# Performance work log

Measured on AMD Instinct MI355X. Metric: run time of the kernel, lower is better.

The kernel has to match this reference:

```python
import jax, jax.numpy as jnp
import numpy as np

T, B, D, H = 1024, 8, 1024, 16
HD = D // H  # head_dim = 64


def setup_inputs() -> dict:
    key = jax.random.key(0)
    ks = jax.random.split(key, 11)
    s = 1.0 / np.sqrt(D)
    return {
        "query": jax.random.normal(ks[0], (T, B, D), jnp.float32),
        "key": jax.random.normal(ks[1], (T, B, D), jnp.float32),
        "value": jax.random.normal(ks[2], (T, B, D), jnp.float32),
        "Wq": jax.random.normal(ks[3], (D, D), jnp.float32) * s,
        "bq": jax.random.normal(ks[4], (D,), jnp.float32) * s,
        "Wk": jax.random.normal(ks[5], (D, D), jnp.float32) * s,
        "bk": jax.random.normal(ks[6], (D,), jnp.float32) * s,
        "Wv": jax.random.normal(ks[7], (D, D), jnp.float32) * s,
        "bv": jax.random.normal(ks[8], (D,), jnp.float32) * s,
        "Wo": jax.random.normal(ks[9], (D, D), jnp.float32) * s,
        "bo": jax.random.normal(ks[10], (D,), jnp.float32) * s,
    }


def reference(query, key, value, Wq, bq, Wk, bk, Wv, bv, Wo, bo):
    # query/key/value: (T, B, D) seq-first, as in nn.MultiheadAttention
    t, b, d = query.shape
    scale = HD ** -0.5
    # projections (torch Linear: x @ W.T + b), split into heads -> (B, H, T, HD)
    q = (query @ Wq.T + bq).reshape(t, b, H, HD).transpose(1, 2, 0, 3)
    k = (key @ Wk.T + bk).reshape(t, b, H, HD).transpose(1, 2, 0, 3)
    v = (value @ Wv.T + bv).reshape(t, b, H, HD).transpose(1, 2, 0, 3)
    # full (B, H, T, T) scores, matching the module's explicit materialization
    attn = jnp.einsum('bhtd,bhsd->bhts', q, k) * scale
    attn = jax.nn.softmax(attn, axis=-1)
    # (B, H, T, HD) -> (T, B, D)
    out = jnp.einsum('bhts,bhsd->bhtd', attn, v)
    out = out.transpose(2, 0, 1, 3).reshape(t, b, d)
    return out @ Wo.T + bo
```

## Files before the change

kernel.cpp:

```cpp
#include <hip/hip_runtime.h>

#define T_SEQ 1024
#define BATCH 8
#define DMODEL 1024
#define NHEAD 16
#define HDIM 64
#define M_ROWS (T_SEQ * BATCH)
#define QSCALE (0.125f * 1.44269504088896f)

typedef unsigned short ushort_t;
typedef __attribute__((ext_vector_type(8))) short short8;
typedef __attribute__((ext_vector_type(4))) float f32x4;

#define G2L16(g, l) __builtin_amdgcn_global_load_lds(                      \
    (const __attribute__((address_space(1))) void*)(g),                    \
    (__attribute__((address_space(3))) void*)(l), 16, 0, 0)

#define SBAR()   __builtin_amdgcn_s_barrier()
#define LGKM0()  asm volatile("s_waitcnt lgkmcnt(0)" ::: "memory")
#define SCHEDB() __builtin_amdgcn_sched_barrier(0)

static __device__ __forceinline__ ushort_t f2bf(float f) {
    unsigned int u = __builtin_bit_cast(unsigned int, f);
    u += 0x7FFFu + ((u >> 16) & 1u);
    return (ushort_t)(u >> 16);
}

#if __has_builtin(__builtin_amdgcn_cvt_pk_bf16_f32)
typedef __attribute__((ext_vector_type(2))) __bf16 bf16x2_t;
static __device__ __forceinline__ unsigned pk2(float lo, float hi) {
    bf16x2_t r = __builtin_amdgcn_cvt_pk_bf16_f32(lo, hi);
    return __builtin_bit_cast(unsigned, r);
}
#else
static __device__ __forceinline__ unsigned pk2(float lo, float hi) {
    return (unsigned)f2bf(lo) | ((unsigned)f2bf(hi) << 16);
}
#endif

#if __has_builtin(__builtin_amdgcn_exp2f)
#define EXP2F(x) __builtin_amdgcn_exp2f(x)
#else
#define EXP2F(x) exp2f(x)
#endif

__global__ __launch_bounds__(256) void cast_all_bf16(
    const float4* __restrict__ s0, const float4* __restrict__ s1,
    const float4* __restrict__ s2, const float4* __restrict__ s3,
    const float4* __restrict__ s4, const float4* __restrict__ s5,
    const float4* __restrict__ s6,
    uint2* __restrict__ d0, uint2* __restrict__ d1, uint2* __restrict__ d2,
    uint2* __restrict__ d3, uint2* __restrict__ d4, uint2* __restrict__ d5,
    uint2* __restrict__ d6, int n4big, int n4small)
{
    const int y = blockIdx.y;
    const int n4 = (y < 3) ? n4big : n4small;
    const int i = blockIdx.x * 256 + threadIdx.x;
    if (i >= n4) return;
    const float4* s; uint2* d;
    switch (y) {
        case 0: s = s0; d = d0; break;
        case 1: s = s1; d = d1; break;
        case 2: s = s2; d = d2; break;
        case 3: s = s3; d = d3; break;
        case 4: s = s4; d = d4; break;
        case 5: s = s5; d = d5; break;
        default: s = s6; d = d6; break;
    }
    float4 v = s[i];
    uint2 o; o.x = pk2(v.x, v.y); o.y = pk2(v.z, v.w);
    d[i] = o;
}

template<bool OUT_BF16>
__global__ __launch_bounds__(256, 4) void gemm_bt_mfma(
    const ushort_t* __restrict__ A, const ushort_t* __restrict__ Wbase,
    const float* __restrict__ bias0, const float* __restrict__ bias1,
    const float* __restrict__ bias2, void* __restrict__ Yv,
    int N, int K, float scale0)
{
    __shared__ ushort_t As[128 * 64];
    __shared__ ushort_t Bs[128 * 64];

    const int tid  = threadIdx.x;
    const int lane = tid & 63;
    const int quad = lane >> 4;
    const int l16  = lane & 15;
    const int w    = tid >> 6;
    const int wm   = w >> 1;
    const int wn   = w & 1;

    const int nwg = gridDim.x * gridDim.y;
    const int lin = blockIdx.y * gridDim.x + blockIdx.x;
    const int t   = (lin & 7) * (nwg >> 3) + (lin >> 3);
    const int bn  = t & 7;
    const int bmg = t >> 3;

    const int sel = bmg >> 6;
    const ushort_t* Wb = Wbase + (size_t)sel * N * K;
    const float* bias = (sel == 0) ? bias0 : (sel == 1) ? bias1 : bias2;
    const float scale = (sel == 0) ? scale0 : 1.0f;

    const int srow_in = lane >> 3;
    const int sch     = lane & 7;

    const f32x4 zero4 = {0.f, 0.f, 0.f, 0.f};
    f32x4 acc[4][4];
#pragma unroll
    for (int i = 0; i < 4; i++)
#pragma unroll
        for (int j = 0; j < 4; j++) acc[i][j] = zero4;

    for (int k0 = 0; k0 < K; k0 += 64) {
        __syncthreads();
#pragma unroll
        for (int u = 0; u < 4; u++) {
            int seg = w * 4 + u;
            int row = seg * 8 + srow_in;
            int chs = sch ^ (row & 7);
            G2L16(&A [(size_t)(bmg * 128 + row) * K + k0 + chs * 8],
                  (char*)As + seg * 1024);
            G2L16(&Wb[(size_t)(bn  * 128 + row) * K + k0 + chs * 8],
                  (char*)Bs + seg * 1024);
        }
        __syncthreads();

#pragma unroll
        for (int ks = 0; ks < 2; ks++) {
            short8 af[4], bfr[4];
#pragma unroll
            for (int i = 0; i < 4; i++) {
                int row = wm * 64 + i * 16 + l16;
                af[i] = *(const short8*)&As[row * 64 + (((ks * 4 + quad) ^ (row & 7)) * 8)];
            }
#pragma unroll
            for (int j = 0; j < 4; j++) {
                int row = wn * 64 + j * 16 + l16;
                bfr[j] = *(const short8*)&Bs[row * 64 + (((ks * 4 + quad) ^ (row & 7)) * 8)];
            }
#pragma unroll
            for (int i = 0; i < 4; i++)
#pragma unroll
                for (int j = 0; j < 4; j++)
                    acc[i][j] = __builtin_amdgcn_mfma_f32_16x16x32_bf16(
                        af[i], bfr[j], acc[i][j], 0, 0, 0);
        }
    }

    float bj[4];
#pragma unroll
    for (int j = 0; j < 4; j++) bj[j] = bias[bn * 128 + wn * 64 + j * 16 + l16];
#pragma unroll
    for (int i = 0; i < 4; i++) {
#pragma unroll
        for (int r = 0; r < 4; r++) {
            size_t row = (size_t)(bmg * 128 + wm * 64 + i * 16 + quad * 4 + r);
#pragma unroll
            for (int j = 0; j < 4; j++) {
                int col = bn * 128 + wn * 64 + j * 16 + l16;
                float v = (acc[i][j][r] + bj[j]) * scale;
                if (OUT_BF16) ((ushort_t*)Yv)[row * N + col] = f2bf(v);
                else          ((float*)   Yv)[row * N + col] = v;
            }
        }
    }
}

__global__ __launch_bounds__(256) void transpose_v(
    const ushort_t* __restrict__ Vp, ushort_t* __restrict__ Vt)
{
    __shared__ ushort_t Ts[64][72];
    const int tid = threadIdx.x;
    const int t0 = blockIdx.x * 64;
    const int bh = blockIdx.y;
    const int b = bh >> 4, h = bh & 15;

#pragma unroll
    for (int u = 0; u < 2; u++) {
        int e = u * 256 + tid;
        int row = e >> 3, ch = (e & 7) * 8;
        uint4 v = *(const uint4*)&Vp[((size_t)(t0 + row) * BATCH + b) * DMODEL + h * 64 + ch];
        *(uint4*)&Ts[row][ch] = v;
    }
    __syncthreads();
#pragma unroll
    for (int u = 0; u < 2; u++) {
        int e = u * 256 + tid;
        int d = e >> 3, tc = (e & 7) * 8;
        uint4 o;
        o.x = (unsigned)Ts[tc + 0][d] | ((unsigned)Ts[tc + 1][d] << 16);
        o.y = (unsigned)Ts[tc + 2][d] | ((unsigned)Ts[tc + 3][d] << 16);
        o.z = (unsigned)Ts[tc + 4][d] | ((unsigned)Ts[tc + 5][d] << 16);
        o.w = (unsigned)Ts[tc + 6][d] | ((unsigned)Ts[tc + 7][d] << 16);
        *(uint4*)&Vt[((size_t)(bh * 64 + d)) * T_SEQ + t0 + tc] = o;
    }
}

__global__ __launch_bounds__(256, 3) void attn_mfma(
    const ushort_t* __restrict__ Qp, const ushort_t* __restrict__ Kp,
    const ushort_t* __restrict__ VtG, ushort_t* __restrict__ Ao)
{
    __shared__ ushort_t Ks[2][64 * 64];
    __shared__ ushort_t Vs[2][64 * 64];
    __shared__ ushort_t Pl[4][32][72];

    const int tid  = threadIdx.x;
    const int lane = tid & 63;
    const int w    = tid >> 6;
    const int quad = lane >> 4;
    const int l16  = lane & 15;
    const int bid  = blockIdx.x;
    const int qb   = bid >> 7;
    const int bh   = bid & 127;
    const int b    = bh >> 4, h = bh & 15;
    const int hoff = h * 64;
    const int q0   = qb * 128 + w * 32;

    const int srow_in = lane >> 3;
    const int sch     = lane & 7;

    short8 qf[2][2];
#pragma unroll
    for (int rt = 0; rt < 2; rt++)
#pragma unroll
        for (int ks = 0; ks < 2; ks++)
            qf[rt][ks] = *(const short8*)&Qp[((size_t)(q0 + rt * 16 + l16) * BATCH + b) * DMODEL
                                             + hoff + ks * 32 + quad * 8];

    short8 ones;
#pragma unroll
    for (int i = 0; i < 8; i++) ones[i] = (short)0x3F80;

    const f32x4 zero4 = {0.f, 0.f, 0.f, 0.f};
    f32x4 oacc[2][4], lacc[2];
#pragma unroll
    for (int rt = 0; rt < 2; rt++) {
        lacc[rt] = zero4;
#pragma unroll
        for (int c = 0; c < 4; c++) oacc[rt][c] = zero4;
    }

#define STAGE_KV(s0_, buf)                                                       \
    do {                                                                         \
        _Pragma("unroll")                                                        \
        for (int u = 0; u < 2; u++) {                                            \
            int seg = w * 2 + u;                                                 \
            int row = seg * 8 + srow_in;                                         \
            int chs = sch ^ (row & 7);                                           \
            G2L16(&Kp[((size_t)((s0_) + row) * BATCH + b) * DMODEL + hoff + chs * 8], \
                  (char*)&Ks[buf][0] + seg * 1024);                              \
            G2L16(&VtG[((size_t)(bh * 64 + row)) * T_SEQ + (s0_) + chs * 8],     \
                  (char*)&Vs[buf][0] + seg * 1024);                              \
        }                                                                        \
    } while (0)

    STAGE_KV(0, 0);

    for (int it = 0; it < 16; ++it) {
        const int cur = it & 1;

        asm volatile("s_waitcnt vmcnt(0)" ::: "memory");
        SBAR();
        SCHEDB();
        if (it + 1 < 16) STAGE_KV((it + 1) * 64, cur ^ 1);

        f32x4 sacc[2][4];
#pragma unroll
        for (int rt = 0; rt < 2; rt++)
#pragma unroll
            for (int c = 0; c < 4; c++) sacc[rt][c] = zero4;
        __builtin_amdgcn_s_setprio(1);
#pragma unroll
        for (int c = 0; c < 4; c++) {
            int row = c * 16 + l16;
#pragma unroll
            for (int ks = 0; ks < 2; ks++) {
                short8 kf = *(const short8*)&Ks[cur][row * 64 + (((ks * 4 + quad) ^ (row & 7)) * 8)];
#pragma unroll
                for (int rt = 0; rt < 2; rt++)
                    sacc[rt][c] = __builtin_amdgcn_mfma_f32_16x16x32_bf16(
                        kf, qf[rt][ks], sacc[rt][c], 0, 0, 0);
            }
        }
        __builtin_amdgcn_s_setprio(0);

#pragma unroll
        for (int rt = 0; rt < 2; rt++)
#pragma unroll
            for (int c = 0; c < 4; c++) {
                uint2 pv;
                pv.x = pk2(EXP2F(sacc[rt][c][0]), EXP2F(sacc[rt][c][1]));
                pv.y = pk2(EXP2F(sacc[rt][c][2]), EXP2F(sacc[rt][c][3]));
                *(uint2*)&Pl[w][rt * 16 + l16][c * 16 + quad * 4] = pv;
            }

        short8 pf[2][2];
#pragma unroll
        for (int rt = 0; rt < 2; rt++)
#pragma unroll
            for (int ks = 0; ks < 2; ks++)
                pf[rt][ks] = *(const short8*)&Pl[w][rt * 16 + l16][ks * 32 + quad * 8];

#pragma unroll
        for (int rt = 0; rt < 2; rt++)
#pragma unroll
            for (int ks = 0; ks < 2; ks++)
                lacc[rt] = __builtin_amdgcn_mfma_f32_16x16x32_bf16(
                    ones, pf[rt][ks], lacc[rt], 0, 0, 0);

        __builtin_amdgcn_s_setprio(1);
#pragma unroll
        for (int dt = 0; dt < 4; dt++) {
            int row = dt * 16 + l16;
#pragma unroll
            for (int ks = 0; ks < 2; ks++) {
                short8 vf = *(const short8*)&Vs[cur][row * 64 + (((ks * 4 + quad) ^ (row & 7)) * 8)];
#pragma unroll
                for (int rt = 0; rt < 2; rt++)
                    oacc[rt][dt] = __builtin_amdgcn_mfma_f32_16x16x32_bf16(
                        vf, pf[rt][ks], oacc[rt][dt], 0, 0, 0);
            }
        }
        __builtin_amdgcn_s_setprio(0);

        LGKM0();
    }
#undef STAGE_KV

#pragma unroll
    for (int rt = 0; rt < 2; rt++) {
        float inv = 1.f / lacc[rt][0];
#pragma unroll
        for (int dt = 0; dt < 4; dt++) {
            uint2 ov;
            ov.x = pk2(oacc[rt][dt][0] * inv, oacc[rt][dt][1] * inv);
            ov.y = pk2(oacc[rt][dt][2] * inv, oacc[rt][dt][3] * inv);
            *(uint2*)&Pl[w][rt * 16 + l16][dt * 16 + quad * 4] = ov;
        }
    }
#pragma unroll
    for (int it = 0; it < 4; it++) {
        int row = it * 8 + (lane >> 3);
        int ch  = lane & 7;
        uint4 val = *(const uint4*)&Pl[w][row][ch * 8];
        *(uint4*)&Ao[((size_t)(q0 + row) * BATCH + b) * DMODEL + hoff + ch * 8] = val;
    }
}

extern "C" void kernel_launch(void* const* d_in, const int* in_sizes, int n_in,
                              void* d_out, int out_size, void* d_ws, size_t ws_size,
                              hipStream_t stream)
{
    const float* q  = (const float*)d_in[0];
    const float* k  = (const float*)d_in[1];
    const float* v  = (const float*)d_in[2];
    const float* Wq = (const float*)d_in[3];
    const float* bq = (const float*)d_in[4];
    const float* Wk = (const float*)d_in[5];
    const float* bk = (const float*)d_in[6];
    const float* Wv = (const float*)d_in[7];
    const float* bv = (const float*)d_in[8];
    const float* Wo = (const float*)d_in[9];
    const float* bo = (const float*)d_in[10];

    ushort_t* ws = (ushort_t*)d_ws;
    const size_t E = (size_t)M_ROWS * DMODEL;
    const size_t EW = (size_t)DMODEL * DMODEL;
    ushort_t* qb  = ws;
    ushort_t* kb  = ws + E;
    ushort_t* vb  = ws + 2 * E;
    ushort_t* Qp  = ws + 3 * E;
    ushort_t* Kp  = ws + 4 * E;
    ushort_t* Vp  = ws + 5 * E;
    ushort_t* Wqb = ws + 6 * E;
    ushort_t* Wkb = Wqb + EW;
    ushort_t* Wvb = Wkb + EW;
    ushort_t* Wob = Wvb + EW;
    ushort_t* Vt  = qb;
    ushort_t* Aob = kb;

    const int n4_in = (int)(E / 4);
    const int n4_w  = (int)(EW / 4);
    cast_all_bf16<<<dim3(n4_in / 256, 7), 256, 0, stream>>>(
        (const float4*)q, (const float4*)k, (const float4*)v,
        (const float4*)Wq, (const float4*)Wk, (const float4*)Wv, (const float4*)Wo,
        (uint2*)qb, (uint2*)kb, (uint2*)vb,
        (uint2*)Wqb, (uint2*)Wkb, (uint2*)Wvb, (uint2*)Wob,
        n4_in, n4_w);

    gemm_bt_mfma<true><<<dim3(DMODEL / 128, 3 * M_ROWS / 128), 256, 0, stream>>>(
        qb, Wqb, bq, bk, bv, Qp, DMODEL, DMODEL, QSCALE);

    transpose_v<<<dim3(T_SEQ / 64, BATCH * NHEAD), 256, 0, stream>>>(Vp, Vt);

    attn_mfma<<<dim3(8 * 128), 256, 0, stream>>>(Qp, Kp, Vt, Aob);

    gemm_bt_mfma<false><<<dim3(DMODEL / 128, M_ROWS / 128), 256, 0, stream>>>(
        Aob, Wob, bo, bo, bo, d_out, DMODEL, DMODEL, 1.0f);
}
```

Before: 306.5 us.

## Shrink P staging buffer with XOR swizzle and raise attention occupancy to 4 blocks

Halves the per-wave P staging buffer in LDS from 32x72 to 16x64 by processing the two row tiles one after another, and replaces the padding with an XOR swizzle to avoid bank conflicts. V fragments are loaded once into registers and reused across both row tiles. Launch bounds go from 3 to 4 blocks per CU, so more blocks fit within the LDS and register budget. The risks are extra register pressure from holding the V fragments under the tighter occupancy target, and more serialization between the P writes and reads.

```diff
diff --git a/kernel.cpp b/kernel.cpp
--- a/kernel.cpp
+++ b/kernel.cpp
@@ -196,13 +196,13 @@
     }
 }
 
-__global__ __launch_bounds__(256, 3) void attn_mfma(
+__global__ __launch_bounds__(256, 4) void attn_mfma(
     const ushort_t* __restrict__ Qp, const ushort_t* __restrict__ Kp,
     const ushort_t* __restrict__ VtG, ushort_t* __restrict__ Ao)
 {
     __shared__ ushort_t Ks[2][64 * 64];
     __shared__ ushort_t Vs[2][64 * 64];
-    __shared__ ushort_t Pl[4][32][72];
+    __shared__ ushort_t Pl[4][16][64];
 
     const int tid  = threadIdx.x;
     const int lane = tid & 63;
@@ -218,6 +218,7 @@
 
     const int srow_in = lane >> 3;
     const int sch     = lane & 7;
+    const int plswz   = (l16 & 7) << 1;
 
     short8 qf[2][2];
 #pragma unroll
@@ -284,44 +285,48 @@
         }
         __builtin_amdgcn_s_setprio(0);
 
+        uint2 pk[2][4];
 #pragma unroll
         for (int rt = 0; rt < 2; rt++)
 #pragma unroll
             for (int c = 0; c < 4; c++) {
-                uint2 pv;
-                pv.x = pk2(EXP2F(sacc[rt][c][0]), EXP2F(sacc[rt][c][1]));
-                pv.y = pk2(EXP2F(sacc[rt][c][2]), EXP2F(sacc[rt][c][3]));
-                *(uint2*)&Pl[w][rt * 16 + l16][c * 16 + quad * 4] = pv;
-            }
-
-        short8 pf[2][2];
-#pragma unroll
-        for (int rt = 0; rt < 2; rt++)
-#pragma unroll
-            for (int ks = 0; ks < 2; ks++)
-                pf[rt][ks] = *(const short8*)&Pl[w][rt * 16 + l16][ks * 32 + quad * 8];
-
-#pragma unroll
-        for (int rt = 0; rt < 2; rt++)
+                pk[rt][c].x = pk2(EXP2F(sacc[rt][c][0]), EXP2F(sacc[rt][c][1]));
+                pk[rt][c].y = pk2(EXP2F(sacc[rt][c][2]), EXP2F(sacc[rt][c][3]));
+            }
+
+        short8 vf[4][2];
+#pragma unroll
+        for (int rt = 0; rt < 2; rt++) {
+#pragma unroll
+            for (int c = 0; c < 4; c++) {
+                int slot = (c * 4 + quad) ^ plswz;
+                *(uint2*)((char*)&Pl[w][l16][0] + slot * 8) = pk[rt][c];
+            }
+            short8 pf[2];
+#pragma unroll
+            for (int ks = 0; ks < 2; ks++) {
+                int slot = (ks * 8 + quad * 2) ^ plswz;
+                pf[ks] = *(const short8*)((const char*)&Pl[w][l16][0] + slot * 8);
+            }
 #pragma unroll
             for (int ks = 0; ks < 2; ks++)
                 lacc[rt] = __builtin_amdgcn_mfma_f32_16x16x32_bf16(
-                    ones, pf[rt][ks], lacc[rt], 0, 0, 0);
-
-        __builtin_amdgcn_s_setprio(1);
-#pragma unroll
-        for (int dt = 0; dt < 4; dt++) {
-            int row = dt * 16 + l16;
-#pragma unroll
-            for (int ks = 0; ks < 2; ks++) {
-                short8 vf = *(const short8*)&Vs[cur][row * 64 + (((ks * 4 + quad) ^ (row & 7)) * 8)];
-#pragma unroll
-                for (int rt = 0; rt < 2; rt++)
+                    ones, pf[ks], lacc[rt], 0, 0, 0);
+            __builtin_amdgcn_s_setprio(1);
+#pragma unroll
+            for (int dt = 0; dt < 4; dt++) {
+                int row = dt * 16 + l16;
+#pragma unroll
+                for (int ks = 0; ks < 2; ks++) {
+                    if (rt == 0)
+                        vf[dt][ks] = *(const short8*)&Vs[cur][row * 64 +
+                                     (((ks * 4 + quad) ^ (row & 7)) * 8)];
                     oacc[rt][dt] = __builtin_amdgcn_mfma_f32_16x16x32_bf16(
-                        vf, pf[rt][ks], oacc[rt][dt], 0, 0, 0);
-            }
-        }
-        __builtin_amdgcn_s_setprio(0);
+                        vf[dt][ks], pf[ks], oacc[rt][dt], 0, 0, 0);
+                }
+            }
+            __builtin_amdgcn_s_setprio(0);
+        }
 
         LGKM0();
     }
@@ -335,15 +340,17 @@
             uint2 ov;
             ov.x = pk2(oacc[rt][dt][0] * inv, oacc[rt][dt][1] * inv);
             ov.y = pk2(oacc[rt][dt][2] * inv, oacc[rt][dt][3] * inv);
-            *(uint2*)&Pl[w][rt * 16 + l16][dt * 16 + quad * 4] = ov;
-        }
-    }
-#pragma unroll
-    for (int it = 0; it < 4; it++) {
-        int row = it * 8 + (lane >> 3);
-        int ch  = lane & 7;
-        uint4 val = *(const uint4*)&Pl[w][row][ch * 8];
-        *(uint4*)&Ao[((size_t)(q0 + row) * BATCH + b) * DMODEL + hoff + ch * 8] = val;
+            int slot = (dt * 4 + quad) ^ plswz;
+            *(uint2*)((char*)&Pl[w][l16][0] + slot * 8) = ov;
+        }
+#pragma unroll
+        for (int it2 = 0; it2 < 2; it2++) {
+            int row = it2 * 8 + (lane >> 3);
+            int ch  = lane & 7;
+            int slot = (ch * 2) ^ ((row & 7) << 1);
+            uint4 val = *(const uint4*)((const char*)&Pl[w][row][0] + slot * 8);
+            *(uint4*)&Ao[((size_t)(q0 + rt * 16 + row) * BATCH + b) * DMODEL + hoff + ch * 8] = val;
+        }
     }
 }
 
```

Result: no change. 306.4 us (-0.0%).
